# Performance work log

Hardware: AMD Instinct MI355X
Metric: run time of the kernel (lower is better)

Reference implementation:

```python
import jax, jax.numpy as jnp
import numpy as np

B, S, HID = 2, 2048, 4096
NH, NKV, HD = 32, 8, 128
SLIDING_WINDOW = 1024
ROPE_THETA = 10000.0


def setup_inputs() -> dict:
    key = jax.random.key(0)
    ks = jax.random.split(key, 6)
    hidden_states = jax.random.normal(ks[0], (B, S, HID), dtype=jnp.float32)
    attention_mask = jnp.ones((B, S), dtype=jnp.int32)
    position_ids = jnp.broadcast_to(jnp.arange(S, dtype=jnp.int32)[None, :], (B, S))
    sc = 1.0 / np.sqrt(HID)
    q_w = jax.random.normal(ks[1], (HID, NH * HD), dtype=jnp.float32) * sc
    k_w = jax.random.normal(ks[2], (HID, NKV * HD), dtype=jnp.float32) * sc
    v_w = jax.random.normal(ks[3], (HID, NKV * HD), dtype=jnp.float32) * sc
    o_w = jax.random.normal(ks[4], (NH * HD, HID), dtype=jnp.float32) * sc
    return {"hidden_states": hidden_states, "attention_mask": attention_mask,
            "position_ids": position_ids, "q_w": q_w, "k_w": k_w, "v_w": v_w, "o_w": o_w}


def _rotate_half(x):
    return jnp.concatenate((-x[..., x.shape[-1] // 2:], x[..., : x.shape[-1] // 2]), axis=-1)


def _rope_sincos(position_ids):
    # inv_freq over even dims of head_dim; emb = concat(freqs, freqs)
    inv_freq = 1.0 / ROPE_THETA ** (jnp.arange(0, HD, 2, dtype=jnp.float32) / HD)
    freqs = position_ids.astype(jnp.float32)[..., None] * inv_freq  # [B,S,HD/2]
    emb = jnp.concatenate((freqs, freqs), axis=-1)                  # [B,S,HD]
    # broadcast over heads axis: [B,S,1,HD]
    return jnp.sin(emb)[:, :, None, :], jnp.cos(emb)[:, :, None, :]


def reference(hidden_states, attention_mask, position_ids, q_w, k_w, v_w, o_w):
    b, q_len, _ = hidden_states.shape
    n_rep = NH // NKV

    q = (hidden_states @ q_w).reshape(b, q_len, NH, HD)
    k = (hidden_states @ k_w).reshape(b, q_len, NKV, HD)
    v = (hidden_states @ v_w).reshape(b, q_len, NKV, HD)

    sin_pos, cos_pos = _rope_sincos(position_ids)
    q = q * cos_pos + _rotate_half(q) * sin_pos
    k = k * cos_pos + _rotate_half(k) * sin_pos

    # GQA: repeat kv heads (repeat_interleave along head axis)
    k = jnp.repeat(k, n_rep, axis=2)  # [B,S,NH,HD]
    v = jnp.repeat(v, n_rep, axis=2)

    # sliding-window causal mask: j <= i and j >= i - sliding_window
    i = jnp.arange(q_len)[:, None]
    j = jnp.arange(q_len)[None, :]
    band = (j <= i) & (j >= i - SLIDING_WINDOW)           # [Q,K]
    mask = band[None, None] & (attention_mask[:, None, None, :] > 0)  # [B,1,Q,K]

    bias = jnp.where(mask, 0.0, jnp.finfo(jnp.float32).min)

    scale = 1.0 / jnp.sqrt(jnp.asarray(HD, dtype=jnp.float32))
    scores = jnp.einsum('bqhd,bkhd->bhqk', q, k) * scale + bias
    attn_weights = jax.nn.softmax(scores, axis=-1)
    attn_out = jnp.einsum('bhqk,bkhd->bqhd', attn_weights, v)
    attn_out = attn_out.reshape(b, q_len, HID)
    return attn_out @ o_w
```

## Files before the change

kernel.cpp:

```cpp
#include <hip/hip_runtime.h>
#include <stdint.h>
#include <stddef.h>

typedef __bf16 bf16x8 __attribute__((ext_vector_type(8)));
typedef short short8 __attribute__((ext_vector_type(8)));
typedef float floatx4 __attribute__((ext_vector_type(4)));
typedef unsigned short ushort4v __attribute__((ext_vector_type(4)));

__device__ __forceinline__ unsigned short f2bf(float f){
  unsigned int u = __float_as_uint(f);
  u += 0x7fffu + ((u >> 16) & 1u);
  return (unsigned short)(u >> 16);
}
__device__ __forceinline__ float bf2f(unsigned short s){
  return __uint_as_float(((unsigned int)s) << 16);
}
__device__ __forceinline__ void gl2lds16(const void* g, void* l){
  __builtin_amdgcn_global_load_lds((const __attribute__((address_space(1))) void*)g,
                                   (__attribute__((address_space(3))) void*)l, 16, 0, 0);
}

__global__ __launch_bounds__(256) void conv_f32_bf16(const float* __restrict__ in,
                                                     unsigned short* __restrict__ out){
  int t = blockIdx.x * 256 + threadIdx.x;
  floatx4 v = *(const floatx4*)(in + (size_t)t * 4);
  ushort4v o;
#pragma unroll
  for (int j = 0; j < 4; ++j) o[j] = f2bf(v[j]);
  *(ushort4v*)(out + (size_t)t * 4) = o;
}

__global__ __launch_bounds__(256) void transpose_cvt(const float* __restrict__ in,
                                                     unsigned short* __restrict__ out,
                                                     int Kd, int Nd){
  __shared__ __align__(16) unsigned short tile[64 * 80];
  int n0 = blockIdx.x * 64, k0 = blockIdx.y * 64;
  int t = threadIdx.x;
#pragma unroll
  for (int it = 0; it < 2; ++it){
    int rr = (t >> 3) + it * 32;
    int cc = t & 7;
    const float* src = in + (size_t)(k0 + rr) * Nd + n0 + cc * 8;
    floatx4 a = *(const floatx4*)src;
    floatx4 b = *(const floatx4*)(src + 4);
    short8 s;
#pragma unroll
    for (int j = 0; j < 4; ++j){ s[j] = (short)f2bf(a[j]); s[j + 4] = (short)f2bf(b[j]); }
    *(short8*)&tile[rr * 80 + cc * 8] = s;
  }
  __syncthreads();
#pragma unroll
  for (int it = 0; it < 2; ++it){
    int nr = (t >> 3) + it * 32;
    int kc = t & 7;
    short8 v;
#pragma unroll
    for (int j = 0; j < 8; ++j) v[j] = (short)tile[(kc * 8 + j) * 80 + nr];
    *(short8*)(out + (size_t)(n0 + nr) * Kd + k0 + kc * 8) = v;
  }
}

__global__ __launch_bounds__(256, 2) void gemm_bt(
    const unsigned short* __restrict__ A,
    const unsigned short* __restrict__ Wq,
    const unsigned short* __restrict__ Wk,
    const unsigned short* __restrict__ Wv,
    unsigned short* __restrict__ oQ,
    unsigned short* __restrict__ oK,
    unsigned short* __restrict__ oVt,
    float* __restrict__ oF, int f32out)
{
  __shared__ __align__(16) unsigned short As[128 * 64];
  __shared__ __align__(16) unsigned short Bs[128 * 64];
  const int tid = threadIdx.x;
  const int w = tid >> 6, lane = tid & 63, quad = lane >> 4, l15 = lane & 15;
  const int wm64 = (w >> 1) * 64, wn64 = (w & 1) * 64;
  const int m0 = blockIdx.y * 128;
  const int n0 = blockIdx.x * 128;

  const unsigned short* Wsrc;
  int nb, region;
  if (n0 < 4096)      { Wsrc = Wq; nb = n0;        region = 0; }
  else if (n0 < 5120) { Wsrc = Wk; nb = n0 - 4096; region = 1; }
  else                { Wsrc = Wv; nb = n0 - 5120; region = 2; }

  floatx4 acc[4][4];
#pragma unroll
  for (int i = 0; i < 4; ++i)
#pragma unroll
    for (int j = 0; j < 4; ++j) acc[i][j] = (floatx4){0.f, 0.f, 0.f, 0.f};

  const int rsub = lane >> 3, csub = lane & 7;

  for (int k0 = 0; k0 < 4096; k0 += 64){
#pragma unroll
    for (int i = 0; i < 4; ++i){
      int u = i * 4 + w;
      int r = u * 8 + rsub;
      gl2lds16(A    + ((size_t)(m0 + r) << 12) + k0 + ((csub ^ (r & 7)) << 3), (char*)As + u * 1024);
      gl2lds16(Wsrc + ((size_t)(nb + r) << 12) + k0 + ((csub ^ (r & 7)) << 3), (char*)Bs + u * 1024);
    }
    __syncthreads();
#pragma unroll
    for (int ks = 0; ks < 2; ++ks){
      bf16x8 af[4], bfr[4];
#pragma unroll
      for (int mt = 0; mt < 4; ++mt){
        int r = wm64 + mt * 16 + l15;
        int kc = ks * 4 + quad;
        af[mt] = *(const bf16x8*)&As[r * 64 + ((kc ^ (r & 7)) << 3)];
      }
#pragma unroll
      for (int nt = 0; nt < 4; ++nt){
        int r = wn64 + nt * 16 + l15;
        int kc = ks * 4 + quad;
        bfr[nt] = *(const bf16x8*)&Bs[r * 64 + ((kc ^ (r & 7)) << 3)];
      }
#pragma unroll
      for (int mt = 0; mt < 4; ++mt)
#pragma unroll
        for (int nt = 0; nt < 4; ++nt)
          acc[mt][nt] = __builtin_amdgcn_mfma_f32_16x16x32_bf16(af[mt], bfr[nt], acc[mt][nt], 0, 0, 0);
    }
    __syncthreads();
  }

  if (region == 0){
    if (f32out){
#pragma unroll
      for (int mt = 0; mt < 4; ++mt)
#pragma unroll
        for (int nt = 0; nt < 4; ++nt){
          int gn = n0 + wn64 + nt * 16 + l15;
#pragma unroll
          for (int rr = 0; rr < 4; ++rr){
            int gm = m0 + wm64 + mt * 16 + quad * 4 + rr;
            oF[((size_t)gm << 12) + gn] = acc[mt][nt][rr];
          }
        }
    } else {
#pragma unroll
      for (int mt = 0; mt < 4; ++mt)
#pragma unroll
        for (int nt = 0; nt < 4; ++nt){
          int gn = n0 + wn64 + nt * 16 + l15;
#pragma unroll
          for (int rr = 0; rr < 4; ++rr){
            int gm = m0 + wm64 + mt * 16 + quad * 4 + rr;
            oQ[((size_t)gm << 12) + gn] = f2bf(acc[mt][nt][rr]);
          }
        }
    }
  } else if (region == 1){
#pragma unroll
    for (int mt = 0; mt < 4; ++mt)
#pragma unroll
      for (int nt = 0; nt < 4; ++nt){
        int gn = n0 - 4096 + wn64 + nt * 16 + l15;
#pragma unroll
        for (int rr = 0; rr < 4; ++rr){
          int gm = m0 + wm64 + mt * 16 + quad * 4 + rr;
          oK[((size_t)gm << 10) + gn] = f2bf(acc[mt][nt][rr]);
        }
      }
  } else {
#pragma unroll
    for (int mt = 0; mt < 4; ++mt){
      int gm0 = m0 + wm64 + mt * 16 + quad * 4;
      int b = gm0 >> 11, s0 = gm0 & 2047;
#pragma unroll
      for (int nt = 0; nt < 4; ++nt){
        int dg = n0 - 5120 + wn64 + nt * 16 + l15;
        int kvh = dg >> 7, d = dg & 127;
        ushort4v pk;
#pragma unroll
        for (int rr = 0; rr < 4; ++rr) pk[rr] = f2bf(acc[mt][nt][rr]);
        *(ushort4v*)(oVt + (((size_t)(b * 8 + kvh) * 128 + d) * 2048 + s0)) = pk;
      }
    }
  }
}

__global__ void rope_apply_k(unsigned short* __restrict__ Qb, unsigned short* __restrict__ Kb,
                             const int* __restrict__ pos){
  int t = blockIdx.x * 256 + threadIdx.x;
  unsigned short* base;
  int row, ch;
  bool isq = (t < 1048576);
  if (isq){ row = t >> 8; int c = t & 255; base = Qb + ((size_t)row << 12) + (c >> 3) * 128; ch = c & 7; }
  else { int t2 = t - 1048576; row = t2 >> 6; int c = t2 & 63; base = Kb + ((size_t)row << 10) + (c >> 3) * 128; ch = c & 7; }
  float p = (float)pos[row];
  const float qs = 0.08838834764831845f * 1.44269504088896340736f;
  float sc_out = isq ? qs : 1.0f;
  int d0 = ch * 8;
  short8 x0 = *(short8*)(base + d0);
  short8 x1 = *(short8*)(base + d0 + 64);
  short8 y0, y1;
#pragma unroll
  for (int j = 0; j < 8; ++j){
    float ang = p * exp2f(-(float)(d0 + j) * 0.20762050593045952f);
    float sn = sinf(ang), cs = cosf(ang);
    float a  = bf2f((unsigned short)x0[j]);
    float bb = bf2f((unsigned short)x1[j]);
    y0[j] = (short)f2bf((a * cs - bb * sn) * sc_out);
    y1[j] = (short)f2bf((bb * cs + a * sn) * sc_out);
  }
  *(short8*)(base + d0)      = y0;
  *(short8*)(base + d0 + 64) = y1;
}

__global__ __launch_bounds__(256, 2) void flash_swa(
    const unsigned short* __restrict__ Q,
    const unsigned short* __restrict__ K,
    const unsigned short* __restrict__ Vt,
    const int* __restrict__ amask,
    unsigned short* __restrict__ attn)
{
  __shared__ __align__(16) unsigned short Kl[2][64 * 128];
  __shared__ __align__(16) unsigned short Vl[2][128 * 64];
  __shared__ __align__(16) unsigned short Pl[4 * 16 * 64];
  const int qt = blockIdx.x, h = blockIdx.y, b = blockIdx.z;
  const int kv = h >> 2;
  const int tid = threadIdx.x, w = tid >> 6, lane = tid & 63, quad = lane >> 4, l15 = lane & 15;
  const int q0 = qt * 64;

  bool anybad = false;
  {
    const int* ap = amask + b * 2048 + lane * 32;
#pragma unroll
    for (int i = 0; i < 8; ++i){
      int4 mv = *(const int4*)(ap + i * 4);
      anybad |= (mv.x <= 0) | (mv.y <= 0) | (mv.z <= 0) | (mv.w <= 0);
    }
  }
  const bool allv = (__ballot(anybad) == 0ull);

  bf16x8 qf[4];
  {
    const unsigned short* qbase = Q + (((size_t)(b * 2048 + q0 + w * 16 + l15)) << 12) + h * 128;
#pragma unroll
    for (int ks = 0; ks < 4; ++ks) qf[ks] = *(const bf16x8*)(qbase + ks * 32 + quad * 8);
  }
  floatx4 acco[8];
#pragma unroll
  for (int i = 0; i < 8; ++i) acco[i] = (floatx4){0.f, 0.f, 0.f, 0.f};
  float m_i[4] = {-1e30f, -1e30f, -1e30f, -1e30f};
  float l_i[4] = {0.f, 0.f, 0.f, 0.f};

  const int ts = (qt >= 16) ? (qt - 16) : 0;

#define STAGE_KV(JT, BUF)                                                                  \
  {                                                                                        \
    const int k0s = (JT) * 64;                                                             \
    _Pragma("unroll")                                                                      \
    for (int i_ = 0; i_ < 4; ++i_){                                                        \
      int u_ = i_ * 4 + w;                                                                 \
      int r_ = u_ * 4 + (lane >> 4);                                                       \
      int c_ = lane & 15;                                                                  \
      gl2lds16(K + (((size_t)(b * 2048 + k0s + r_)) << 10) + kv * 128 + ((c_ ^ (r_ & 15)) << 3), \
               (char*)Kl[BUF] + u_ * 1024);                                                \
    }                                                                                      \
    _Pragma("unroll")                                                                      \
    for (int i_ = 0; i_ < 4; ++i_){                                                        \
      int u_ = i_ * 4 + w;                                                                 \
      int d_ = u_ * 8 + (lane >> 3);                                                       \
      int c_ = lane & 7;                                                                   \
      gl2lds16(Vt + ((size_t)(b * 8 + kv) * 128 + d_) * 2048 + k0s + ((c_ ^ (d_ & 7)) << 3), \
               (char*)Vl[BUF] + u_ * 1024);                                                \
    }                                                                                      \
  }

  STAGE_KV(ts, 0);
  __syncthreads();

  int cur = 0;
  for (int jt = ts; jt <= qt; ++jt){
    const int k0 = jt * 64;
    if (jt < qt) STAGE_KV(jt + 1, cur ^ 1);

    const unsigned short* Klc = Kl[cur];
    const unsigned short* Vlc = Vl[cur];

    floatx4 accs[4];
#pragma unroll
    for (int i = 0; i < 4; ++i) accs[i] = (floatx4){0.f, 0.f, 0.f, 0.f};
    __builtin_amdgcn_s_setprio(1);
#pragma unroll
    for (int ks = 0; ks < 4; ++ks)
#pragma unroll
      for (int nt = 0; nt < 4; ++nt){
        int r = nt * 16 + l15;
        int kc = ks * 4 + quad;
        bf16x8 kf = *(const bf16x8*)&Klc[r * 128 + ((kc ^ (r & 15)) << 3)];
        accs[nt] = __builtin_amdgcn_mfma_f32_16x16x32_bf16(qf[ks], kf, accs[nt], 0, 0, 0);
      }
    __builtin_amdgcn_s_setprio(0);

    bool slow = (jt == qt) || ((qt - jt) == 16) || (!allv);
    if (slow){
#pragma unroll
      for (int nt = 0; nt < 4; ++nt){
        int j = k0 + nt * 16 + l15;
        int mk = amask[b * 2048 + j];
#pragma unroll
        for (int rr = 0; rr < 4; ++rr){
          int irow = q0 + w * 16 + quad * 4 + rr;
          bool valid = (j <= irow) && (j >= irow - 1024) && (mk > 0);
          accs[nt][rr] = valid ? accs[nt][rr] : -1e30f;
        }
      }
    }

    float vmax[4]; float need = 0.f;
#pragma unroll
    for (int rr = 0; rr < 4; ++rr){
      float v = fmaxf(fmaxf(accs[0][rr], accs[1][rr]), fmaxf(accs[2][rr], accs[3][rr]));
#pragma unroll
      for (int d_ = 1; d_ < 16; d_ <<= 1) v = fmaxf(v, __shfl_xor(v, d_));
      vmax[rr] = v;
      need = fmaxf(need, v - m_i[rr]);
    }
    if (!__all(need <= 8.0f)){
#pragma unroll
      for (int rr = 0; rr < 4; ++rr){
        float mnew = fmaxf(m_i[rr], vmax[rr]);
        float alpha = exp2f(m_i[rr] - mnew);
        m_i[rr] = mnew;
        l_i[rr] *= alpha;
#pragma unroll
        for (int n2 = 0; n2 < 8; ++n2) acco[n2][rr] *= alpha;
      }
    }
#pragma unroll
    for (int rr = 0; rr < 4; ++rr){
      float rs = 0.f;
#pragma unroll
      for (int nt = 0; nt < 4; ++nt){
        float p = exp2f(accs[nt][rr] - m_i[rr]);
        accs[nt][rr] = p;
        rs += p;
      }
#pragma unroll
      for (int d_ = 1; d_ < 16; d_ <<= 1) rs += __shfl_xor(rs, d_);
      l_i[rr] += rs;
    }
#pragma unroll
    for (int nt = 0; nt < 4; ++nt)
#pragma unroll
      for (int rr = 0; rr < 4; ++rr){
        int row = quad * 4 + rr;
        Pl[w * 1024 + row * 64 + ((nt * 16 + l15) ^ ((row & 7) << 3))] = f2bf(accs[nt][rr]);
      }
    __builtin_amdgcn_s_setprio(1);
#pragma unroll
    for (int ks2 = 0; ks2 < 2; ++ks2){
      bf16x8 pf = *(const bf16x8*)&Pl[w * 1024 + l15 * 64 + ((ks2 * 32 + quad * 8) ^ ((l15 & 7) << 3))];
#pragma unroll
      for (int n2 = 0; n2 < 8; ++n2){
        int d = n2 * 16 + l15;
        int sc = ks2 * 4 + quad;
        bf16x8 vf = *(const bf16x8*)&Vlc[d * 64 + ((sc ^ (d & 7)) << 3)];
        acco[n2] = __builtin_amdgcn_mfma_f32_16x16x32_bf16(pf, vf, acco[n2], 0, 0, 0);
      }
    }
    __builtin_amdgcn_s_setprio(0);
    __syncthreads();
    cur ^= 1;
  }
#undef STAGE_KV

  float inv[4];
#pragma unroll
  for (int rr = 0; rr < 4; ++rr) inv[rr] = 1.f / l_i[rr];
#pragma unroll
  for (int n2 = 0; n2 < 8; ++n2)
#pragma unroll
    for (int rr = 0; rr < 4; ++rr){
      size_t off = (((size_t)(b * 2048 + q0 + w * 16 + quad * 4 + rr)) << 12) + h * 128 + n2 * 16 + l15;
      attn[off] = f2bf(acco[n2][rr] * inv[rr]);
    }
}

extern "C" void kernel_launch(void* const* d_in, const int* in_sizes, int n_in,
                              void* d_out, int out_size, void* d_ws, size_t ws_size,
                              hipStream_t stream){
  const float* hidden = (const float*)d_in[0];
  const int* amask = (const int*)d_in[1];
  const int* pos   = (const int*)d_in[2];
  const float* qw = (const float*)d_in[3];
  const float* kw = (const float*)d_in[4];
  const float* vw = (const float*)d_in[5];
  const float* ow = (const float*)d_in[6];

  char* ws = (char*)d_ws;
  unsigned short* hb   = (unsigned short*)(ws + 0);
  unsigned short* qt   = (unsigned short*)(ws + 33554432);
  unsigned short* kt   = (unsigned short*)(ws + 67108864);
  unsigned short* vtw  = (unsigned short*)(ws + 75497472);
  unsigned short* Qb   = (unsigned short*)(ws + 83886080);
  unsigned short* Kb   = (unsigned short*)(ws + 117440512);
  unsigned short* Vtb  = (unsigned short*)(ws + 125829120);
  unsigned short* ot   = hb;
  unsigned short* attn = qt;
  float* outp = (float*)d_out;

  hipLaunchKernelGGL(conv_f32_bf16, dim3(16384), dim3(256), 0, stream, hidden, hb);
  hipLaunchKernelGGL(transpose_cvt, dim3(64, 64), dim3(256), 0, stream, qw, qt, 4096, 4096);
  hipLaunchKernelGGL(transpose_cvt, dim3(16, 64), dim3(256), 0, stream, kw, kt, 4096, 1024);
  hipLaunchKernelGGL(transpose_cvt, dim3(16, 64), dim3(256), 0, stream, vw, vtw, 4096, 1024);
  hipLaunchKernelGGL(gemm_bt, dim3(48, 32), dim3(256), 0, stream,
                     hb, qt, kt, vtw, Qb, Kb, Vtb, (float*)nullptr, 0);
  hipLaunchKernelGGL(transpose_cvt, dim3(64, 64), dim3(256), 0, stream, ow, ot, 4096, 4096);
  hipLaunchKernelGGL(rope_apply_k, dim3(5120), dim3(256), 0, stream, Qb, Kb, pos);
  hipLaunchKernelGGL(flash_swa, dim3(32, 32, 2), dim3(256), 0, stream, Qb, Kb, Vtb, amask, attn);
  hipLaunchKernelGGL(gemm_bt, dim3(32, 32), dim3(256), 0, stream,
                     attn, ot, ot, ot, nullptr, nullptr, nullptr, outp, 1);
}
```

Measured before the change: 764.1 us.

## Rework flash attention to 128-query tiles with 32x32 MFMA and staged output writes

The flash SWA kernel now handles 128 query rows per block (32 per wave) instead of 64, so each K/V tile staged into LDS is reused by twice as many queries. It also switches from 16x16x32 to 32x32x16 MFMAs, and computes S^T = K·Q^T so each lane owns a single query row, which removes the shuffle reductions for row max and sum. Output is transposed through LDS and written as 16-byte vector stores. In exchange the grid is halved, and some waves sit idle on the edge tiles that fall outside their own window, which wastes work.

```diff
diff --git a/kernel.cpp b/kernel.cpp
--- a/kernel.cpp
+++ b/kernel.cpp
@@ -5,7 +5,9 @@
 typedef __bf16 bf16x8 __attribute__((ext_vector_type(8)));
 typedef short short8 __attribute__((ext_vector_type(8)));
 typedef float floatx4 __attribute__((ext_vector_type(4)));
+typedef float f32x16 __attribute__((ext_vector_type(16)));
 typedef unsigned short ushort4v __attribute__((ext_vector_type(4)));
+typedef unsigned int uint2v __attribute__((ext_vector_type(2)));
 
 __device__ __forceinline__ unsigned short f2bf(float f){
   unsigned int u = __float_as_uint(f);
@@ -218,11 +220,15 @@
 {
   __shared__ __align__(16) unsigned short Kl[2][64 * 128];
   __shared__ __align__(16) unsigned short Vl[2][128 * 64];
-  __shared__ __align__(16) unsigned short Pl[4 * 16 * 64];
-  const int qt = blockIdx.x, h = blockIdx.y, b = blockIdx.z;
+  __shared__ __align__(16) unsigned int   Pl[4][1024];
+  const int h = blockIdx.y, b = blockIdx.z;
   const int kv = h >> 2;
-  const int tid = threadIdx.x, w = tid >> 6, lane = tid & 63, quad = lane >> 4, l15 = lane & 15;
-  const int q0 = qt * 64;
+  const int tid = threadIdx.x, w = tid >> 6, lane = tid & 63;
+  const int l31 = lane & 31, hi = lane >> 5, hi4 = hi << 2;
+  const int qb = blockIdx.x * 128;
+  const int t0 = qb >> 6;
+  const int qw0 = qb + w * 32;
+  const int aw = t0 + (w >> 1);
 
   bool anybad = false;
   {
@@ -235,19 +241,22 @@
   }
   const bool allv = (__ballot(anybad) == 0ull);
 
-  bf16x8 qf[4];
+  bf16x8 qf[8];
   {
-    const unsigned short* qbase = Q + (((size_t)(b * 2048 + q0 + w * 16 + l15)) << 12) + h * 128;
-#pragma unroll
-    for (int ks = 0; ks < 4; ++ks) qf[ks] = *(const bf16x8*)(qbase + ks * 32 + quad * 8);
-  }
-  floatx4 acco[8];
-#pragma unroll
-  for (int i = 0; i < 8; ++i) acco[i] = (floatx4){0.f, 0.f, 0.f, 0.f};
-  float m_i[4] = {-1e30f, -1e30f, -1e30f, -1e30f};
-  float l_i[4] = {0.f, 0.f, 0.f, 0.f};
-
-  const int ts = (qt >= 16) ? (qt - 16) : 0;
+    const unsigned short* qbase = Q + (((size_t)(b * 2048 + qw0 + l31)) << 12) + h * 128;
+#pragma unroll
+    for (int ds = 0; ds < 8; ++ds) qf[ds] = *(const bf16x8*)(qbase + ds * 16 + hi * 8);
+  }
+
+  f32x16 acco[4];
+#pragma unroll
+  for (int i = 0; i < 4; ++i)
+#pragma unroll
+    for (int j = 0; j < 16; ++j) acco[i][j] = 0.f;
+  float m_i = -1e30f, l_i = 0.f;
+
+  const int jb0 = (t0 >= 16) ? (t0 - 16) : 0;
+  const int jtend = t0 + 1;
 
 #define STAGE_KV(JT, BUF)                                                                  \
   {                                                                                        \
@@ -270,115 +279,147 @@
     }                                                                                      \
   }
 
-  STAGE_KV(ts, 0);
+  STAGE_KV(jb0, 0);
   __syncthreads();
 
+  unsigned int* Pw = &Pl[w][0];
   int cur = 0;
-  for (int jt = ts; jt <= qt; ++jt){
-    const int k0 = jt * 64;
-    if (jt < qt) STAGE_KV(jt + 1, cur ^ 1);
-
-    const unsigned short* Klc = Kl[cur];
-    const unsigned short* Vlc = Vl[cur];
-
-    floatx4 accs[4];
-#pragma unroll
-    for (int i = 0; i < 4; ++i) accs[i] = (floatx4){0.f, 0.f, 0.f, 0.f};
-    __builtin_amdgcn_s_setprio(1);
-#pragma unroll
-    for (int ks = 0; ks < 4; ++ks)
-#pragma unroll
-      for (int nt = 0; nt < 4; ++nt){
-        int r = nt * 16 + l15;
-        int kc = ks * 4 + quad;
-        bf16x8 kf = *(const bf16x8*)&Klc[r * 128 + ((kc ^ (r & 15)) << 3)];
-        accs[nt] = __builtin_amdgcn_mfma_f32_16x16x32_bf16(qf[ks], kf, accs[nt], 0, 0, 0);
-      }
-    __builtin_amdgcn_s_setprio(0);
-
-    bool slow = (jt == qt) || ((qt - jt) == 16) || (!allv);
-    if (slow){
-#pragma unroll
-      for (int nt = 0; nt < 4; ++nt){
-        int j = k0 + nt * 16 + l15;
-        int mk = amask[b * 2048 + j];
-#pragma unroll
-        for (int rr = 0; rr < 4; ++rr){
-          int irow = q0 + w * 16 + quad * 4 + rr;
-          bool valid = (j <= irow) && (j >= irow - 1024) && (mk > 0);
-          accs[nt][rr] = valid ? accs[nt][rr] : -1e30f;
-        }
-      }
-    }
-
-    float vmax[4]; float need = 0.f;
-#pragma unroll
-    for (int rr = 0; rr < 4; ++rr){
-      float v = fmaxf(fmaxf(accs[0][rr], accs[1][rr]), fmaxf(accs[2][rr], accs[3][rr]));
-#pragma unroll
-      for (int d_ = 1; d_ < 16; d_ <<= 1) v = fmaxf(v, __shfl_xor(v, d_));
-      vmax[rr] = v;
-      need = fmaxf(need, v - m_i[rr]);
-    }
-    if (!__all(need <= 8.0f)){
-#pragma unroll
-      for (int rr = 0; rr < 4; ++rr){
-        float mnew = fmaxf(m_i[rr], vmax[rr]);
-        float alpha = exp2f(m_i[rr] - mnew);
-        m_i[rr] = mnew;
-        l_i[rr] *= alpha;
-#pragma unroll
-        for (int n2 = 0; n2 < 8; ++n2) acco[n2][rr] *= alpha;
-      }
-    }
-#pragma unroll
-    for (int rr = 0; rr < 4; ++rr){
-      float rs = 0.f;
-#pragma unroll
-      for (int nt = 0; nt < 4; ++nt){
-        float p = exp2f(accs[nt][rr] - m_i[rr]);
-        accs[nt][rr] = p;
-        rs += p;
-      }
-#pragma unroll
-      for (int d_ = 1; d_ < 16; d_ <<= 1) rs += __shfl_xor(rs, d_);
-      l_i[rr] += rs;
-    }
-#pragma unroll
-    for (int nt = 0; nt < 4; ++nt)
-#pragma unroll
-      for (int rr = 0; rr < 4; ++rr){
-        int row = quad * 4 + rr;
-        Pl[w * 1024 + row * 64 + ((nt * 16 + l15) ^ ((row & 7) << 3))] = f2bf(accs[nt][rr]);
-      }
-    __builtin_amdgcn_s_setprio(1);
-#pragma unroll
-    for (int ks2 = 0; ks2 < 2; ++ks2){
-      bf16x8 pf = *(const bf16x8*)&Pl[w * 1024 + l15 * 64 + ((ks2 * 32 + quad * 8) ^ ((l15 & 7) << 3))];
-#pragma unroll
-      for (int n2 = 0; n2 < 8; ++n2){
-        int d = n2 * 16 + l15;
-        int sc = ks2 * 4 + quad;
-        bf16x8 vf = *(const bf16x8*)&Vlc[d * 64 + ((sc ^ (d & 7)) << 3)];
-        acco[n2] = __builtin_amdgcn_mfma_f32_16x16x32_bf16(pf, vf, acco[n2], 0, 0, 0);
-      }
-    }
-    __builtin_amdgcn_s_setprio(0);
+  for (int jt = jb0; jt <= jtend; ++jt){
+    if (jt < jtend) STAGE_KV(jt + 1, cur ^ 1);
+
+    const bool active = (jt >= aw - 16) && (jt <= aw);
+    if (active){
+      const int k0 = jt * 64;
+      const unsigned short* Klc = Kl[cur];
+      const unsigned short* Vlc = Vl[cur];
+
+      f32x16 ps[2];
+#pragma unroll
+      for (int kb = 0; kb < 2; ++kb)
+#pragma unroll
+        for (int j = 0; j < 16; ++j) ps[kb][j] = 0.f;
+
+      __builtin_amdgcn_s_setprio(1);
+#pragma unroll
+      for (int ds = 0; ds < 8; ++ds){
+#pragma unroll
+        for (int kb = 0; kb < 2; ++kb){
+          int r = kb * 32 + l31;
+          bf16x8 kf = *(const bf16x8*)&Klc[r * 128 + (((ds * 2 + hi) ^ (r & 15)) << 3)];
+          ps[kb] = __builtin_amdgcn_mfma_f32_32x32x16_bf16(kf, qf[ds], ps[kb], 0, 0, 0);
+        }
+      }
+      __builtin_amdgcn_s_setprio(0);
+
+      const bool slow = (jt == aw) || (jt == aw - 16) || (!allv);
+      if (slow){
+        unsigned long long mb = __ballot(amask[b * 2048 + k0 + lane] > 0);
+        int irow = qw0 + l31;
+#pragma unroll
+        for (int kb = 0; kb < 2; ++kb)
+#pragma unroll
+          for (int reg = 0; reg < 16; ++reg){
+            int jv = k0 + kb * 32 + (reg & 3) + 8 * (reg >> 2) + hi4;
+            bool valid = (jv <= irow) && (jv >= irow - 1024) &&
+                         (((mb >> (jv & 63)) & 1ull) != 0ull);
+            ps[kb][reg] = valid ? ps[kb][reg] : -1e30f;
+          }
+      }
+
+      float t16[16];
+#pragma unroll
+      for (int r = 0; r < 16; ++r) t16[r] = fmaxf(ps[0][r], ps[1][r]);
+      float t8[8];
+#pragma unroll
+      for (int r = 0; r < 8; ++r) t8[r] = fmaxf(t16[r], t16[r + 8]);
+      float t4[4];
+#pragma unroll
+      for (int r = 0; r < 4; ++r) t4[r] = fmaxf(t8[r], t8[r + 4]);
+      float vm = fmaxf(fmaxf(t4[0], t4[1]), fmaxf(t4[2], t4[3]));
+      float vmax = fmaxf(vm, __shfl_xor(vm, 32));
+
+      if (!__all(vmax - m_i <= 8.0f)){
+        float mnew = fmaxf(m_i, vmax);
+        float alpha = exp2f(m_i - mnew);
+        m_i = mnew;
+        l_i *= alpha;
+#pragma unroll
+        for (int db = 0; db < 4; ++db) acco[db] *= alpha;
+      }
+
+#pragma unroll
+      for (int kb = 0; kb < 2; ++kb)
+#pragma unroll
+        for (int reg = 0; reg < 16; ++reg) ps[kb][reg] = exp2f(ps[kb][reg] - m_i);
+
+      float s16[16];
+#pragma unroll
+      for (int r = 0; r < 16; ++r) s16[r] = ps[0][r] + ps[1][r];
+      float s8[8];
+#pragma unroll
+      for (int r = 0; r < 8; ++r) s8[r] = s16[r] + s16[r + 8];
+      float s4[4];
+#pragma unroll
+      for (int r = 0; r < 4; ++r) s4[r] = s8[r] + s8[r + 4];
+      float sm = (s4[0] + s4[1]) + (s4[2] + s4[3]);
+      l_i += sm + __shfl_xor(sm, 32);
+
+#pragma unroll
+      for (int kb = 0; kb < 2; ++kb)
+#pragma unroll
+        for (int g = 0; g < 4; ++g){
+          unsigned p0 = (unsigned)f2bf(ps[kb][g * 4 + 0]) | ((unsigned)f2bf(ps[kb][g * 4 + 1]) << 16);
+          unsigned p1 = (unsigned)f2bf(ps[kb][g * 4 + 2]) | ((unsigned)f2bf(ps[kb][g * 4 + 3]) << 16);
+          int ch = (kb * 4 + g) ^ (l31 & 7);
+          uint2v pv_; pv_[0] = p0; pv_[1] = p1;
+          *(uint2v*)&Pw[l31 * 32 + ch * 4 + hi * 2] = pv_;
+        }
+      bf16x8 pa[4];
+#pragma unroll
+      for (int ks = 0; ks < 4; ++ks)
+        pa[ks] = *(const bf16x8*)&Pw[l31 * 32 + (((ks * 2 + hi) ^ (l31 & 7)) << 2)];
+
+      __builtin_amdgcn_s_setprio(1);
+#pragma unroll
+      for (int ks = 0; ks < 4; ++ks){
+#pragma unroll
+        for (int db = 0; db < 4; ++db){
+          int d = db * 32 + l31;
+          bf16x8 vf = *(const bf16x8*)&Vlc[d * 64 + (((ks * 2 + hi) ^ (d & 7)) << 3)];
+          acco[db] = __builtin_amdgcn_mfma_f32_32x32x16_bf16(vf, pa[ks], acco[db], 0, 0, 0);
+        }
+      }
+      __builtin_amdgcn_s_setprio(0);
+    }
+
     __syncthreads();
     cur ^= 1;
   }
 #undef STAGE_KV
 
-  float inv[4];
-#pragma unroll
-  for (int rr = 0; rr < 4; ++rr) inv[rr] = 1.f / l_i[rr];
-#pragma unroll
-  for (int n2 = 0; n2 < 8; ++n2)
-#pragma unroll
-    for (int rr = 0; rr < 4; ++rr){
-      size_t off = (((size_t)(b * 2048 + q0 + w * 16 + quad * 4 + rr)) << 12) + h * 128 + n2 * 16 + l15;
-      attn[off] = f2bf(acco[n2][rr] * inv[rr]);
-    }
+  float invl = 1.f / l_i;
+  unsigned short* Ep = ((unsigned short*)Kl) + w * 4096;
+  {
+    const int q = l31;
+#pragma unroll
+    for (int db = 0; db < 4; ++db)
+#pragma unroll
+      for (int reg = 0; reg < 16; ++reg){
+        int dc = db * 4 + (reg >> 2);
+        int dl = (reg & 3) + hi4;
+        Ep[q * 128 + ((dc ^ (q & 15)) << 3) + dl] = f2bf(acco[db][reg] * invl);
+      }
+  }
+  {
+    const int rr_ = lane >> 4, cc = lane & 15;
+#pragma unroll
+    for (int p8 = 0; p8 < 8; ++p8){
+      int q = p8 * 4 + rr_;
+      short8 vv = *(const short8*)&Ep[q * 128 + ((cc ^ (q & 15)) << 3)];
+      size_t off = (((size_t)(b * 2048 + qb + w * 32 + q)) << 12) + h * 128 + cc * 8;
+      *(short8*)(attn + off) = vv;
+    }
+  }
 }
 
 extern "C" void kernel_launch(void* const* d_in, const int* in_sizes, int n_in,
@@ -412,7 +453,7 @@
                      hb, qt, kt, vtw, Qb, Kb, Vtb, (float*)nullptr, 0);
   hipLaunchKernelGGL(transpose_cvt, dim3(64, 64), dim3(256), 0, stream, ow, ot, 4096, 4096);
   hipLaunchKernelGGL(rope_apply_k, dim3(5120), dim3(256), 0, stream, Qb, Kb, pos);
-  hipLaunchKernelGGL(flash_swa, dim3(32, 32, 2), dim3(256), 0, stream, Qb, Kb, Vtb, amask, attn);
+  hipLaunchKernelGGL(flash_swa, dim3(16, 32, 2), dim3(256), 0, stream, Qb, Kb, Vtb, amask, attn);
   hipLaunchKernelGGL(gemm_bt, dim3(32, 32), dim3(256), 0, stream,
                      attn, ot, ot, ot, nullptr, nullptr, nullptr, outp, 1);
 }
```

Measured after the change: 698.8 us. -8.5%, faster.
